# Performance work log

Hardware: AMD Instinct MI355X
Metric: run time of the kernel (lower is better)

Reference implementation:

```python
import jax, jax.numpy as jnp
import numpy as np

N_NODES = 100000


def gcn_conv(x, edge_index, W, b, n_nodes):
    # PyG GCNConv: x' = D^{-1/2} (A + I) D^{-1/2} (x W) + b
    src, dst = edge_index[0], edge_index[1]
    h = x @ W  # linear transform first (in_ch >= out_ch path in PyG)
    # degree with self-loops, computed on target nodes
    deg = jax.ops.segment_sum(jnp.ones_like(dst, dtype=h.dtype), dst,
                              num_segments=n_nodes) + 1.0
    dinv = jax.lax.rsqrt(deg)  # deg >= 1 due to self-loops
    # edge messages: norm_e * h[src]
    norm_e = dinv[src] * dinv[dst]  # [E]
    msg = h[src] * norm_e[:, None]  # [E, out]
    agg = jax.ops.segment_sum(msg, dst, num_segments=n_nodes)
    # self-loop contribution: dinv[i]^2 * h[i]
    out = agg + h * (dinv * dinv)[:, None] + b
    return out


def setup_inputs() -> dict:
    key = jax.random.key(0)
    k1, k2, k3, k4 = jax.random.split(key, 4)
    N, E, F, H, C = N_NODES, 1600000, 128, 64, 32
    x = jax.random.normal(k1, (N, F), dtype=jnp.float32)
    edge_index = jax.random.randint(k2, (2, E), 0, N, dtype=jnp.int64)
    # glorot-style init
    W1 = jax.random.normal(k3, (F, H), dtype=jnp.float32) * (1.0 / np.sqrt(F))
    W2 = jax.random.normal(k4, (H, C), dtype=jnp.float32) * (1.0 / np.sqrt(H))
    b1 = jnp.zeros((H,), dtype=jnp.float32)
    b2 = jnp.zeros((C,), dtype=jnp.float32)
    return {"x": x, "edge_index": edge_index, "W1": W1, "b1": b1,
            "W2": W2, "b2": b2}


def reference(x, edge_index, W1, b1, W2, b2):
    n = x.shape[0]
    h = gcn_conv(x, edge_index, W1, b1, n)
    h = jax.nn.relu(h)
    # dropout is identity in eval mode (reference baseline)
    out = gcn_conv(h, edge_index, W2, b2, n)
    return out
```

## Files before the change

### kernel.cpp

```cpp
#include <hip/hip_runtime.h>
#include <hip/hip_fp16.h>

#define B_HIST 512
#define SHIFT  9

typedef _Float16 f16x8 __attribute__((ext_vector_type(8)));
typedef float f32x4 __attribute__((ext_vector_type(4)));


__global__ __launch_bounds__(256) void p1_hist(const int* __restrict__ dst,
                                               int* __restrict__ histT, int E) {
  __shared__ int h[256];
  const int t = threadIdx.x;
  h[t] = 0;
  __syncthreads();
  const int epb = (E + B_HIST - 1) / B_HIST;
  const int beg = blockIdx.x * epb;
  const int end = min(beg + epb, E);
  for (int e = beg + t; e < end; e += 256)
    atomicAdd(&h[dst[e] >> SHIFT], 1);
  __syncthreads();
  histT[t * B_HIST + blockIdx.x] = h[t];
}

__global__ __launch_bounds__(256) void p2a_colscan(int* __restrict__ histT,
                                                   int* __restrict__ bsum) {
  __shared__ int sdata[256];
  const int bin = blockIdx.x, t = threadIdx.x;
  const int i0 = bin * B_HIST + 2 * t;
  int c0 = histT[i0], c1 = histT[i0 + 1];
  int s = c0 + c1;
  sdata[t] = s;
  __syncthreads();
  for (int off = 1; off < 256; off <<= 1) {
    int x = 0;
    if (t >= off) x = sdata[t - off];
    __syncthreads();
    if (t >= off) sdata[t] += x;
    __syncthreads();
  }
  int excl = sdata[t] - s;
  histT[i0] = excl;
  histT[i0 + 1] = excl + c0;
  if (t == 255) bsum[bin] = sdata[255];
}

__global__ __launch_bounds__(256) void p2b_scan(const int* __restrict__ bsum,
                                                int* __restrict__ colstart) {
  __shared__ int sdata[256];
  const int t = threadIdx.x;
  int v = bsum[t];
  sdata[t] = v;
  __syncthreads();
  for (int off = 1; off < 256; off <<= 1) {
    int x = 0;
    if (t >= off) x = sdata[t - off];
    __syncthreads();
    if (t >= off) sdata[t] += x;
    __syncthreads();
  }
  colstart[t] = sdata[t] - v;
  if (t == 255) colstart[256] = sdata[255];
}

__global__ __launch_bounds__(256) void p3_scatter(const int* __restrict__ src,
                                                  const int* __restrict__ dst,
                                                  const int* __restrict__ histT,
                                                  const int* __restrict__ colstart,
                                                  int* __restrict__ pbuf, int E) {
  __shared__ int cur[256];
  const int t = threadIdx.x;
  cur[t] = colstart[t] + histT[t * B_HIST + blockIdx.x];
  __syncthreads();
  const int epb = (E + B_HIST - 1) / B_HIST;
  const int beg = blockIdx.x * epb;
  const int end = min(beg + epb, E);
  for (int e = beg + t; e < end; e += 256) {
    int d = dst[e];
    int s = src[e];
    int pos = atomicAdd(&cur[d >> SHIFT], 1);
    pbuf[pos] = ((d & 511) << 17) | s;
  }
}

__global__ __launch_bounds__(256) void p4_fine(const int* __restrict__ pbuf,
                                               const int* __restrict__ colstart,
                                               int* __restrict__ rowptr,
                                               float* __restrict__ dinv,
                                               int* __restrict__ ssrc, int N, int NB) {
  __shared__ int cnt[512];
  __shared__ int sdata[256];
  __shared__ int cur[512];
  const int b = blockIdx.x, t = threadIdx.x;
  const int base = colstart[b], endp = colstart[b + 1];
  cnt[2 * t] = 0; cnt[2 * t + 1] = 0;
  __syncthreads();
  for (int i = base + t; i < endp; i += 256)
    atomicAdd(&cnt[pbuf[i] >> 17], 1);
  __syncthreads();
  int c0 = cnt[2 * t], c1 = cnt[2 * t + 1];
  int s = c0 + c1;
  sdata[t] = s;
  __syncthreads();
  for (int off = 1; off < 256; off <<= 1) {
    int x = 0;
    if (t >= off) x = sdata[t - off];
    __syncthreads();
    if (t >= off) sdata[t] += x;
    __syncthreads();
  }
  int excl = sdata[t] - s;
  int e0 = base + excl, e1 = base + excl + c0;
  cur[2 * t] = e0;
  cur[2 * t + 1] = e1;
  int node0 = (b << SHIFT) + 2 * t;
  if (node0 < N) {
    rowptr[node0] = e0;
    dinv[node0] = rsqrtf((float)c0 + 1.0f);
  }
  if (node0 + 1 < N) {
    rowptr[node0 + 1] = e1;
    dinv[node0 + 1] = rsqrtf((float)c1 + 1.0f);
  }
  if (b == NB - 1 && t == 0) rowptr[N] = endp;
  __syncthreads();
  for (int i = base + t; i < endp; i += 256) {
    int p = pbuf[i];
    int pos = atomicAdd(&cur[p >> 17], 1);
    ssrc[pos] = p & 0x1FFFF;
  }
}


template <int COLS, int K, typename XT>
__global__ __launch_bounds__(256) void mfma_gemm(const XT* __restrict__ X,
                                                 const float* __restrict__ W,
                                                 const float* __restrict__ dinv,
                                                 __half* __restrict__ O, int N) {
  constexpr int NKK = K / 32;
  constexpr int NCT = COLS / 16;
  constexpr int RCH = K / 8;
  constexpr int SWM = RCH - 1;
  __shared__ _Float16 xs[64 * K];
  __shared__ _Float16 wb[K * COLS];
  const int t = threadIdx.x;
  const int row0 = blockIdx.x * 64;

  for (int task = t; task < NKK * 4 * COLS; task += 256) {
    int col = task % COLS;
    int kq = task / COLS;
    _Float16 tmp[8];
#pragma unroll
    for (int j = 0; j < 8; ++j)
      tmp[j] = (_Float16)W[(kq * 8 + j) * COLS + col];
    *reinterpret_cast<f16x8*>(&wb[task * 8]) = *reinterpret_cast<const f16x8*>(tmp);
  }
  for (int task = t; task < 64 * RCH; task += 256) {
    int row = task / RCH, c = task % RCH;
    int grow = row0 + row;
    f16x8 hv;
#pragma unroll
    for (int j = 0; j < 8; ++j) hv[j] = (_Float16)0.f;
    if (grow < N) {
      if constexpr (sizeof(XT) == 4) {
        const float4* xr = reinterpret_cast<const float4*>(X + (size_t)grow * K);
        float4 v0 = xr[c * 2], v1 = xr[c * 2 + 1];
        hv[0] = (_Float16)v0.x; hv[1] = (_Float16)v0.y;
        hv[2] = (_Float16)v0.z; hv[3] = (_Float16)v0.w;
        hv[4] = (_Float16)v1.x; hv[5] = (_Float16)v1.y;
        hv[6] = (_Float16)v1.z; hv[7] = (_Float16)v1.w;
      } else {
        hv = reinterpret_cast<const f16x8*>(X + (size_t)grow * K)[c];
      }
    }
    int sc = c ^ (row & SWM);
    *reinterpret_cast<f16x8*>(&xs[row * K + sc * 8]) = hv;
  }
  __syncthreads();

  const int wave = t >> 6, lane = t & 63;
  const int q = lane >> 4, c = lane & 15;
  const int wrow = wave * 16;

  f16x8 bfrag[NKK][NCT];
#pragma unroll
  for (int kk = 0; kk < NKK; ++kk)
#pragma unroll
    for (int ct = 0; ct < NCT; ++ct)
      bfrag[kk][ct] = *reinterpret_cast<const f16x8*>(
          &wb[(size_t)((kk * 4 + q) * COLS + ct * 16 + c) * 8]);

  f32x4 acc[NCT];
#pragma unroll
  for (int ct = 0; ct < NCT; ++ct) acc[ct] = {0.f, 0.f, 0.f, 0.f};

#pragma unroll
  for (int kk = 0; kk < NKK; ++kk) {
    int row = wrow + c;
    int cc = (kk * 4 + q) ^ (row & SWM);
    f16x8 afrag = *reinterpret_cast<const f16x8*>(&xs[row * K + cc * 8]);
#pragma unroll
    for (int ct = 0; ct < NCT; ++ct)
      acc[ct] = __builtin_amdgcn_mfma_f32_16x16x32_f16(afrag, bfrag[kk][ct], acc[ct], 0, 0, 0);
  }

#pragma unroll
  for (int r = 0; r < 4; ++r) {
    int row = row0 + wrow + q * 4 + r;
    if (row < N) {
      float di = dinv[row];
#pragma unroll
      for (int ct = 0; ct < NCT; ++ct)
        O[(size_t)row * COLS + ct * 16 + c] = __float2half(acc[ct][r] * di);
    }
  }
}


__global__ __launch_bounds__(256) void gather64_kernel(const int* __restrict__ rowptr,
                                                       const int* __restrict__ ssrc,
                                                       const float* __restrict__ dinv,
                                                       const uint2* __restrict__ g,
                                                       const float4* __restrict__ bias,
                                                       __half* __restrict__ outb, int N) {
  int node = (blockIdx.x * 256 + threadIdx.x) >> 4;
  int col = threadIdx.x & 15;
  if (node >= N) return;
  int beg = rowptr[node], end = rowptr[node + 1];
  float4 aa0 = {0.f, 0.f, 0.f, 0.f}, aa1 = aa0, aa2 = aa0, aa3 = aa0;
  for (int base = beg; base < end; base += 16) {
    int m = end - base;
    int sv = 0;
    if (col < m) sv = ssrc[base + col];
    uint2 v[16];
#pragma unroll
    for (int u = 0; u < 16; ++u) {
      if (u < m) {
        int s = __shfl(sv, u, 16);
        v[u] = g[(size_t)s * 16 + col];
      }
    }
#pragma unroll
    for (int u = 0; u < 16; ++u) {
      if (u < m) {
        float2 f0 = __half22float2(*(__half2*)&v[u].x);
        float2 f1 = __half22float2(*(__half2*)&v[u].y);
        if ((u & 3) == 0) { aa0.x += f0.x; aa0.y += f0.y; aa0.z += f1.x; aa0.w += f1.y; }
        if ((u & 3) == 1) { aa1.x += f0.x; aa1.y += f0.y; aa1.z += f1.x; aa1.w += f1.y; }
        if ((u & 3) == 2) { aa2.x += f0.x; aa2.y += f0.y; aa2.z += f1.x; aa2.w += f1.y; }
        if ((u & 3) == 3) { aa3.x += f0.x; aa3.y += f0.y; aa3.z += f1.x; aa3.w += f1.y; }
      }
    }
  }
  uint2 vs = g[(size_t)node * 16 + col];
  float2 g01 = __half22float2(*(__half2*)&vs.x);
  float2 g23 = __half22float2(*(__half2*)&vs.y);
  float di = dinv[node];
  float4 bb = bias[col];
  float ox = fmaxf(fmaf(di, (aa0.x + aa1.x) + (aa2.x + aa3.x) + g01.x, bb.x), 0.f);
  float oy = fmaxf(fmaf(di, (aa0.y + aa1.y) + (aa2.y + aa3.y) + g01.y, bb.y), 0.f);
  float oz = fmaxf(fmaf(di, (aa0.z + aa1.z) + (aa2.z + aa3.z) + g23.x, bb.z), 0.f);
  float ow = fmaxf(fmaf(di, (aa0.w + aa1.w) + (aa2.w + aa3.w) + g23.y, bb.w), 0.f);
  union { __half2 h2[2]; uint2 u; } cv;
  cv.h2[0] = __floats2half2_rn(ox, oy);
  cv.h2[1] = __floats2half2_rn(oz, ow);
  reinterpret_cast<uint2*>(outb)[(size_t)node * 16 + col] = cv.u;
}

__global__ __launch_bounds__(256) void gather32_kernel(const int* __restrict__ rowptr,
                                                       const int* __restrict__ ssrc,
                                                       const float* __restrict__ dinv,
                                                       const uint2* __restrict__ g,
                                                       const float4* __restrict__ bias,
                                                       float4* __restrict__ outb, int N) {
  int node = (blockIdx.x * 256 + threadIdx.x) >> 3;
  int col = threadIdx.x & 7;
  if (node >= N) return;
  int beg = rowptr[node], end = rowptr[node + 1];
  float4 aa0 = {0.f, 0.f, 0.f, 0.f}, aa1 = aa0, aa2 = aa0, aa3 = aa0;
  for (int base = beg; base < end; base += 8) {
    int m = end - base;
    int sv = 0;
    if (col < m) sv = ssrc[base + col];
    uint2 v[8];
#pragma unroll
    for (int u = 0; u < 8; ++u) {
      if (u < m) {
        int s = __shfl(sv, u, 8);
        v[u] = g[(size_t)s * 8 + col];
      }
    }
#pragma unroll
    for (int u = 0; u < 8; ++u) {
      if (u < m) {
        float2 f0 = __half22float2(*(__half2*)&v[u].x);
        float2 f1 = __half22float2(*(__half2*)&v[u].y);
        if ((u & 3) == 0) { aa0.x += f0.x; aa0.y += f0.y; aa0.z += f1.x; aa0.w += f1.y; }
        if ((u & 3) == 1) { aa1.x += f0.x; aa1.y += f0.y; aa1.z += f1.x; aa1.w += f1.y; }
        if ((u & 3) == 2) { aa2.x += f0.x; aa2.y += f0.y; aa2.z += f1.x; aa2.w += f1.y; }
        if ((u & 3) == 3) { aa3.x += f0.x; aa3.y += f0.y; aa3.z += f1.x; aa3.w += f1.y; }
      }
    }
  }
  uint2 vs = g[(size_t)node * 8 + col];
  float2 g01 = __half22float2(*(__half2*)&vs.x);
  float2 g23 = __half22float2(*(__half2*)&vs.y);
  float di = dinv[node];
  float4 bb = bias[col];
  float4 o;
  o.x = fmaf(di, (aa0.x + aa1.x) + (aa2.x + aa3.x) + g01.x, bb.x);
  o.y = fmaf(di, (aa0.y + aa1.y) + (aa2.y + aa3.y) + g01.y, bb.y);
  o.z = fmaf(di, (aa0.z + aa1.z) + (aa2.z + aa3.z) + g23.x, bb.z);
  o.w = fmaf(di, (aa0.w + aa1.w) + (aa2.w + aa3.w) + g23.y, bb.w);
  outb[(size_t)node * 8 + col] = o;
}


extern "C" void kernel_launch(void* const* d_in, const int* in_sizes, int n_in,
                              void* d_out, int out_size, void* d_ws, size_t ws_size,
                              hipStream_t stream) {
  const float* x  = (const float*)d_in[0];
  const int*   ei = (const int*)d_in[1];
  const float* W1 = (const float*)d_in[2];
  const float* b1 = (const float*)d_in[3];
  const float* W2 = (const float*)d_in[4];
  const float* b2 = (const float*)d_in[5];
  float* out = (float*)d_out;

  const int H = in_sizes[3];
  const int F = in_sizes[2] / H;
  const int N = in_sizes[0] / F;
  const int E = in_sizes[1] / 2;
  const int* src = ei;
  const int* dst = ei + E;
  const int NB = (N + 511) >> SHIFT;

  char* w = (char*)d_ws;
  auto alloc = [&](size_t bytes) { char* p = w; w += (bytes + 255) & ~(size_t)255; return p; };
  int*     histT    = (int*)alloc((size_t)256 * B_HIST * 4);
  int*     bsum     = (int*)alloc(256 * 4);
  int*     colstart = (int*)alloc(257 * 4);
  int*     pbuf     = (int*)alloc((size_t)E * 4);
  int*     ssrc     = (int*)alloc((size_t)E * 4);
  int*     rowptr   = (int*)alloc((size_t)(N + 1) * 4);
  float*   dinv     = (float*)alloc((size_t)N * 4);
  __half*  g1       = (__half*)alloc((size_t)N * 64 * 2);
  __half*  buf1     = (__half*)alloc((size_t)N * 64 * 2);
  __half*  g2       = (__half*)alloc((size_t)N * 32 * 2);

  p1_hist<<<B_HIST, 256, 0, stream>>>(dst, histT, E);
  p2a_colscan<<<256, 256, 0, stream>>>(histT, bsum);
  p2b_scan<<<1, 256, 0, stream>>>(bsum, colstart);
  p3_scatter<<<B_HIST, 256, 0, stream>>>(src, dst, histT, colstart, pbuf, E);
  p4_fine<<<NB, 256, 0, stream>>>(pbuf, colstart, rowptr, dinv, ssrc, N, NB);

  mfma_gemm<64, 128, float><<<(N + 63) / 64, 256, 0, stream>>>(x, W1, dinv, g1, N);
  gather64_kernel<<<(N * 16 + 255) / 256, 256, 0, stream>>>(rowptr, ssrc, dinv,
      (const uint2*)g1, (const float4*)b1, buf1, N);

  mfma_gemm<32, 64, _Float16><<<(N + 63) / 64, 256, 0, stream>>>(
      (const _Float16*)buf1, W2, dinv, g2, N);
  gather32_kernel<<<(N * 8 + 255) / 256, 256, 0, stream>>>(rowptr, ssrc, dinv,
      (const uint2*)g2, (const float4*)b2, (float4*)out, N);
}
```

Baseline: 140.6 us.

## Store layer-1 features as scaled FP8 and prepack weights once per call

The first GEMM now writes its dinv-scaled output as FP8 (e4m3, pre-scaled by 32) instead of fp16, and the layer-1 gather decodes FP8 with the hardware pack-convert instructions. This halves the bytes moved in the random-access neighbour gather, which dominates the runtime. Weight conversion to fp16 moves out of every GEMM block into small pack kernels, and the layer-2 gather now handles 16 neighbours per iteration for more loads in flight. The cost is a large loss of precision in the hidden features, which may fail tolerance checks, plus two extra kernel launches.

```diff
diff --git a/kernel.cpp b/kernel.cpp
--- a/kernel.cpp
+++ b/kernel.cpp
@@ -6,6 +6,10 @@
 
 typedef _Float16 f16x8 __attribute__((ext_vector_type(8)));
 typedef float f32x4 __attribute__((ext_vector_type(4)));
+typedef float f32x2 __attribute__((ext_vector_type(2)));
+
+#define FP8_SCALE 32.0f
+#define FP8_INV   (1.0f / 32.0f)
 
 
 __global__ __launch_bounds__(256) void p1_hist(const int* __restrict__ dst,
@@ -132,11 +136,26 @@
 }
 
 
-template <int COLS, int K, typename XT>
+template <int COLS, int K>
+__global__ __launch_bounds__(256) void wpack_kernel(const float* __restrict__ W,
+                                                    _Float16* __restrict__ P) {
+  int task = blockIdx.x * 256 + threadIdx.x;
+  if (task >= (K / 8) * COLS) return;
+  int col = task % COLS;
+  int kq = task / COLS;
+  _Float16 tmp[8];
+#pragma unroll
+  for (int j = 0; j < 8; ++j)
+    tmp[j] = (_Float16)W[(kq * 8 + j) * COLS + col];
+  *reinterpret_cast<f16x8*>(&P[task * 8]) = *reinterpret_cast<const f16x8*>(tmp);
+}
+
+
+template <int COLS, int K, typename XT, bool FP8_OUT>
 __global__ __launch_bounds__(256) void mfma_gemm(const XT* __restrict__ X,
-                                                 const float* __restrict__ W,
+                                                 const _Float16* __restrict__ wpk,
                                                  const float* __restrict__ dinv,
-                                                 __half* __restrict__ O, int N) {
+                                                 void* __restrict__ O, int N) {
   constexpr int NKK = K / 32;
   constexpr int NCT = COLS / 16;
   constexpr int RCH = K / 8;
@@ -146,15 +165,8 @@
   const int t = threadIdx.x;
   const int row0 = blockIdx.x * 64;
 
-  for (int task = t; task < NKK * 4 * COLS; task += 256) {
-    int col = task % COLS;
-    int kq = task / COLS;
-    _Float16 tmp[8];
-#pragma unroll
-    for (int j = 0; j < 8; ++j)
-      tmp[j] = (_Float16)W[(kq * 8 + j) * COLS + col];
-    *reinterpret_cast<f16x8*>(&wb[task * 8]) = *reinterpret_cast<const f16x8*>(tmp);
-  }
+  for (int i = t; i < K * COLS / 8; i += 256)
+    *reinterpret_cast<f16x8*>(&wb[i * 8]) = reinterpret_cast<const f16x8*>(wpk)[i];
   for (int task = t; task < 64 * RCH; task += 256) {
     int row = task / RCH, c = task % RCH;
     int grow = row0 + row;
@@ -210,19 +222,26 @@
     if (row < N) {
       float di = dinv[row];
 #pragma unroll
-      for (int ct = 0; ct < NCT; ++ct)
-        O[(size_t)row * COLS + ct * 16 + c] = __float2half(acc[ct][r] * di);
-    }
-  }
-}
-
-
-__global__ __launch_bounds__(256) void gather64_kernel(const int* __restrict__ rowptr,
-                                                       const int* __restrict__ ssrc,
-                                                       const float* __restrict__ dinv,
-                                                       const uint2* __restrict__ g,
-                                                       const float4* __restrict__ bias,
-                                                       __half* __restrict__ outb, int N) {
+      for (int ct = 0; ct < NCT; ++ct) {
+        int col = ct * 16 + c;
+        if constexpr (FP8_OUT) {
+          float v = acc[ct][r] * di * FP8_SCALE;
+          int pk = __builtin_amdgcn_cvt_pk_fp8_f32(v, v, 0, false);
+          ((unsigned char*)O)[(size_t)row * COLS + col] = (unsigned char)(pk & 0xFF);
+        } else {
+          ((__half*)O)[(size_t)row * COLS + col] = __float2half(acc[ct][r] * di);
+        }
+      }
+    }
+  }
+}
+
+__global__ __launch_bounds__(256) void gather64_fp8_kernel(const int* __restrict__ rowptr,
+                                                           const int* __restrict__ ssrc,
+                                                           const float* __restrict__ dinv,
+                                                           const unsigned int* __restrict__ g8,
+                                                           const float4* __restrict__ bias,
+                                                           __half* __restrict__ outb, int N) {
   int node = (blockIdx.x * 256 + threadIdx.x) >> 4;
   int col = threadIdx.x & 15;
   if (node >= N) return;
@@ -232,35 +251,35 @@
     int m = end - base;
     int sv = 0;
     if (col < m) sv = ssrc[base + col];
-    uint2 v[16];
+    unsigned int v[16];
 #pragma unroll
     for (int u = 0; u < 16; ++u) {
       if (u < m) {
         int s = __shfl(sv, u, 16);
-        v[u] = g[(size_t)s * 16 + col];
+        v[u] = g8[(size_t)s * 16 + col];
       }
     }
 #pragma unroll
     for (int u = 0; u < 16; ++u) {
       if (u < m) {
-        float2 f0 = __half22float2(*(__half2*)&v[u].x);
-        float2 f1 = __half22float2(*(__half2*)&v[u].y);
-        if ((u & 3) == 0) { aa0.x += f0.x; aa0.y += f0.y; aa0.z += f1.x; aa0.w += f1.y; }
-        if ((u & 3) == 1) { aa1.x += f0.x; aa1.y += f0.y; aa1.z += f1.x; aa1.w += f1.y; }
-        if ((u & 3) == 2) { aa2.x += f0.x; aa2.y += f0.y; aa2.z += f1.x; aa2.w += f1.y; }
-        if ((u & 3) == 3) { aa3.x += f0.x; aa3.y += f0.y; aa3.z += f1.x; aa3.w += f1.y; }
-      }
-    }
-  }
-  uint2 vs = g[(size_t)node * 16 + col];
-  float2 g01 = __half22float2(*(__half2*)&vs.x);
-  float2 g23 = __half22float2(*(__half2*)&vs.y);
-  float di = dinv[node];
+        f32x2 lo = __builtin_amdgcn_cvt_pk_f32_fp8((int)v[u], false);
+        f32x2 hi = __builtin_amdgcn_cvt_pk_f32_fp8((int)v[u], true);
+        if ((u & 3) == 0) { aa0.x += lo.x; aa0.y += lo.y; aa0.z += hi.x; aa0.w += hi.y; }
+        if ((u & 3) == 1) { aa1.x += lo.x; aa1.y += lo.y; aa1.z += hi.x; aa1.w += hi.y; }
+        if ((u & 3) == 2) { aa2.x += lo.x; aa2.y += lo.y; aa2.z += hi.x; aa2.w += hi.y; }
+        if ((u & 3) == 3) { aa3.x += lo.x; aa3.y += lo.y; aa3.z += hi.x; aa3.w += hi.y; }
+      }
+    }
+  }
+  unsigned int vs = g8[(size_t)node * 16 + col];
+  f32x2 slo = __builtin_amdgcn_cvt_pk_f32_fp8((int)vs, false);
+  f32x2 shi = __builtin_amdgcn_cvt_pk_f32_fp8((int)vs, true);
+  float inv = dinv[node] * FP8_INV;
   float4 bb = bias[col];
-  float ox = fmaxf(fmaf(di, (aa0.x + aa1.x) + (aa2.x + aa3.x) + g01.x, bb.x), 0.f);
-  float oy = fmaxf(fmaf(di, (aa0.y + aa1.y) + (aa2.y + aa3.y) + g01.y, bb.y), 0.f);
-  float oz = fmaxf(fmaf(di, (aa0.z + aa1.z) + (aa2.z + aa3.z) + g23.x, bb.z), 0.f);
-  float ow = fmaxf(fmaf(di, (aa0.w + aa1.w) + (aa2.w + aa3.w) + g23.y, bb.w), 0.f);
+  float ox = fmaxf(fmaf(inv, (aa0.x + aa1.x) + (aa2.x + aa3.x) + slo.x, bb.x), 0.f);
+  float oy = fmaxf(fmaf(inv, (aa0.y + aa1.y) + (aa2.y + aa3.y) + slo.y, bb.y), 0.f);
+  float oz = fmaxf(fmaf(inv, (aa0.z + aa1.z) + (aa2.z + aa3.z) + shi.x, bb.z), 0.f);
+  float ow = fmaxf(fmaf(inv, (aa0.w + aa1.w) + (aa2.w + aa3.w) + shi.y, bb.w), 0.f);
   union { __half2 h2[2]; uint2 u; } cv;
   cv.h2[0] = __floats2half2_rn(ox, oy);
   cv.h2[1] = __floats2half2_rn(oz, ow);
@@ -278,20 +297,28 @@
   if (node >= N) return;
   int beg = rowptr[node], end = rowptr[node + 1];
   float4 aa0 = {0.f, 0.f, 0.f, 0.f}, aa1 = aa0, aa2 = aa0, aa3 = aa0;
-  for (int base = beg; base < end; base += 8) {
+  for (int base = beg; base < end; base += 16) {
     int m = end - base;
-    int sv = 0;
-    if (col < m) sv = ssrc[base + col];
-    uint2 v[8];
+    int sv0 = 0, sv1 = 0;
+    if (col < m) sv0 = ssrc[base + col];
+    if (col + 8 < m) sv1 = ssrc[base + 8 + col];
+    uint2 v[16];
 #pragma unroll
     for (int u = 0; u < 8; ++u) {
       if (u < m) {
-        int s = __shfl(sv, u, 8);
+        int s = __shfl(sv0, u, 8);
         v[u] = g[(size_t)s * 8 + col];
       }
     }
 #pragma unroll
-    for (int u = 0; u < 8; ++u) {
+    for (int u = 8; u < 16; ++u) {
+      if (u < m) {
+        int s = __shfl(sv1, u - 8, 8);
+        v[u] = g[(size_t)s * 8 + col];
+      }
+    }
+#pragma unroll
+    for (int u = 0; u < 16; ++u) {
       if (u < m) {
         float2 f0 = __half22float2(*(__half2*)&v[u].x);
         float2 f1 = __half22float2(*(__half2*)&v[u].y);
@@ -337,16 +364,21 @@
 
   char* w = (char*)d_ws;
   auto alloc = [&](size_t bytes) { char* p = w; w += (bytes + 255) & ~(size_t)255; return p; };
-  int*     histT    = (int*)alloc((size_t)256 * B_HIST * 4);
-  int*     bsum     = (int*)alloc(256 * 4);
-  int*     colstart = (int*)alloc(257 * 4);
-  int*     pbuf     = (int*)alloc((size_t)E * 4);
-  int*     ssrc     = (int*)alloc((size_t)E * 4);
-  int*     rowptr   = (int*)alloc((size_t)(N + 1) * 4);
-  float*   dinv     = (float*)alloc((size_t)N * 4);
-  __half*  g1       = (__half*)alloc((size_t)N * 64 * 2);
-  __half*  buf1     = (__half*)alloc((size_t)N * 64 * 2);
-  __half*  g2       = (__half*)alloc((size_t)N * 32 * 2);
+  int*           histT    = (int*)alloc((size_t)256 * B_HIST * 4);
+  int*           bsum     = (int*)alloc(256 * 4);
+  int*           colstart = (int*)alloc(257 * 4);
+  int*           pbuf     = (int*)alloc((size_t)E * 4);
+  int*           ssrc     = (int*)alloc((size_t)E * 4);
+  int*           rowptr   = (int*)alloc((size_t)(N + 1) * 4);
+  float*         dinv     = (float*)alloc((size_t)N * 4);
+  _Float16*      wp1      = (_Float16*)alloc((size_t)128 * 64 * 2);
+  _Float16*      wp2      = (_Float16*)alloc((size_t)64 * 32 * 2);
+  unsigned char* g1q      = (unsigned char*)alloc((size_t)N * 64);
+  __half*        buf1     = (__half*)alloc((size_t)N * 64 * 2);
+  __half*        g2       = (__half*)alloc((size_t)N * 32 * 2);
+
+  wpack_kernel<64, 128><<<4, 256, 0, stream>>>(W1, wp1);
+  wpack_kernel<32, 64><<<1, 256, 0, stream>>>(W2, wp2);
 
   p1_hist<<<B_HIST, 256, 0, stream>>>(dst, histT, E);
   p2a_colscan<<<256, 256, 0, stream>>>(histT, bsum);
@@ -354,12 +386,12 @@
   p3_scatter<<<B_HIST, 256, 0, stream>>>(src, dst, histT, colstart, pbuf, E);
   p4_fine<<<NB, 256, 0, stream>>>(pbuf, colstart, rowptr, dinv, ssrc, N, NB);
 
-  mfma_gemm<64, 128, float><<<(N + 63) / 64, 256, 0, stream>>>(x, W1, dinv, g1, N);
-  gather64_kernel<<<(N * 16 + 255) / 256, 256, 0, stream>>>(rowptr, ssrc, dinv,
-      (const uint2*)g1, (const float4*)b1, buf1, N);
-
-  mfma_gemm<32, 64, _Float16><<<(N + 63) / 64, 256, 0, stream>>>(
-      (const _Float16*)buf1, W2, dinv, g2, N);
+  mfma_gemm<64, 128, float, true><<<(N + 63) / 64, 256, 0, stream>>>(x, wp1, dinv, g1q, N);
+  gather64_fp8_kernel<<<(N * 16 + 255) / 256, 256, 0, stream>>>(rowptr, ssrc, dinv,
+      (const unsigned int*)g1q, (const float4*)b1, buf1, N);
+
+  mfma_gemm<32, 64, _Float16, false><<<(N + 63) / 64, 256, 0, stream>>>(
+      (const _Float16*)buf1, wp2, dinv, g2, N);
   gather32_kernel<<<(N * 8 + 255) / 256, 256, 0, stream>>>(rowptr, ssrc, dinv,
       (const uint2*)g2, (const float4*)b2, (float4*)out, N);
 }
```

Result: no change. 141.7 us (+0.8%).
